# Kernel tuning notes

Measured on AMD Instinct MI355X. Metric: run time of the kernel, lower is better.

## Reference

```python
import jax, jax.numpy as jnp
import numpy as np

D_MODEL = 256
NUM_TYPES = 7
B, N = 2, 512


def setup_inputs() -> dict:
    key = jax.random.key(0)
    k1, k2, k3 = jax.random.split(key, 3)
    lane_features = jax.random.normal(k1, (B, N, D_MODEL), dtype=jnp.float32)
    # nn.Linear(2D, D): weight [D, 2D], bias [D]; stored transposed for x @ W
    s1 = 1.0 / np.sqrt(2 * D_MODEL)
    W1 = jax.random.uniform(k2, (2 * D_MODEL, D_MODEL), minval=-s1, maxval=s1, dtype=jnp.float32)
    b1 = jnp.zeros((D_MODEL,), dtype=jnp.float32)
    s2 = 1.0 / np.sqrt(D_MODEL)
    W2 = jax.random.uniform(k3, (D_MODEL, NUM_TYPES), minval=-s2, maxval=s2, dtype=jnp.float32)
    b2 = jnp.zeros((NUM_TYPES,), dtype=jnp.float32)
    return {"lane_features": lane_features, "W1": W1, "b1": b1, "W2": W2, "b2": b2}


def reference(lane_features, W1, b1, W2, b2):
    # cat([lane_i, lane_j]) @ W1 == lane_i @ W1[:D] + lane_j @ W1[D:]
    D = lane_features.shape[-1]
    W1a, W1b = W1[:D], W1[D:]
    hi = lane_features @ W1a            # [B, N, D]
    hj = lane_features @ W1b            # [B, N, D]
    h = hi[:, :, None, :] + hj[:, None, :, :] + b1  # [B, N, N, D]
    h = jax.nn.relu(h)                  # dropout is identity at inference
    logits = h @ W2 + b2                # [B, N, N, NUM_TYPES]
    return logits
```

## Files before the change

kernel.cpp:

```cpp
#include <hip/hip_runtime.h>

#define D_MODEL   256
#define NUM_TYPES 7
#define BATCH     2
#define NLANES    512
#define LSTR      264

typedef _Float16  f16x8   __attribute__((ext_vector_type(8)));
typedef float     floatx4 __attribute__((ext_vector_type(4)));


__global__ __launch_bounds__(256) void k1_mfma(
    const float* __restrict__ x, const float* __restrict__ W1,
    const float* __restrict__ b1, const float* __restrict__ W2,
    _Float16* __restrict__ Hi16, _Float16* __restrict__ Hj16,
    _Float16* __restrict__ w2f)
{
    const int tid  = threadIdx.x, lane = tid & 63, w = tid >> 6;
    const int nt   = blockIdx.x;
    const int half = nt >> 4;
    const int nc   = (nt & 15) * 16;
    const int m0   = (blockIdx.y * 4 + w) * 16;
    const int jr   = lane & 15, g = lane >> 4, ks = g * 8;

    const float* xrow = x + (size_t)(m0 + jr) * D_MODEL + ks;
    const float* wb   = W1 + (size_t)(half * D_MODEL + ks) * D_MODEL + nc + jr;

    floatx4 acc = {0.f, 0.f, 0.f, 0.f};
    #pragma unroll
    for (int kc = 0; kc < 8; ++kc) {
        const float4 qa = *(const float4*)(xrow + kc * 32);
        const float4 qb = *(const float4*)(xrow + kc * 32 + 4);
        f16x8 a, bfr;
        a[0] = (_Float16)qa.x; a[1] = (_Float16)qa.y;
        a[2] = (_Float16)qa.z; a[3] = (_Float16)qa.w;
        a[4] = (_Float16)qb.x; a[5] = (_Float16)qb.y;
        a[6] = (_Float16)qb.z; a[7] = (_Float16)qb.w;
        const float* wp = wb + (size_t)(kc * 32) * D_MODEL;
        #pragma unroll
        for (int e = 0; e < 8; ++e)
            bfr[e] = (_Float16)wp[(size_t)e * D_MODEL];
        acc = __builtin_amdgcn_mfma_f32_16x16x32_f16(a, bfr, acc, 0, 0, 0);
    }

    _Float16* Hb = half ? Hj16 : Hi16;
    const float bias = half ? 0.f : b1[nc + jr];
    #pragma unroll
    for (int r = 0; r < 4; ++r)
        Hb[(size_t)(m0 + g * 4 + r) * D_MODEL + nc + jr] = (_Float16)(acc[r] + bias);

    if (nt == 0 && blockIdx.y == 0) {
        #pragma unroll
        for (int s0 = 0; s0 < 2; ++s0) {
            const int s   = tid + s0 * 256;
            const int l2  = s & 63, kc2 = s >> 6;
            const int t2  = l2 & 15, ks2 = (l2 >> 4) * 8;
            f16x8 frag;
            #pragma unroll
            for (int e = 0; e < 8; ++e) {
                const int k = kc2 * 32 + ks2 + e;
                frag[e] = (t2 < NUM_TYPES)
                    ? (_Float16)W2[(size_t)k * NUM_TYPES + t2] : (_Float16)0.f;
            }
            *(f16x8*)(w2f + (size_t)s * 8) = frag;
        }
    }
}

#define COMPUTE_U(H, U)                                                          \
    do {                                                                         \
        _Pragma("unroll")                                                        \
        for (int kc = 0; kc < 4; ++kc) {                                         \
            const f16x8 z = {};                                                  \
            f16x8 s0 = __builtin_elementwise_max(H[kc] + hjr0[kc], z);           \
            acc##U[0] = __builtin_amdgcn_mfma_f32_16x16x32_f16(                  \
                w2h[kc], s0, acc##U[0], 0, 0, 0);                                \
            f16x8 s1 = __builtin_elementwise_max(H[kc] + hjr1[kc], z);           \
            acc##U[1] = __builtin_amdgcn_mfma_f32_16x16x32_f16(                  \
                w2h[kc], s1, acc##U[1], 0, 0, 0);                                \
        }                                                                        \
    } while (0)

__global__ __launch_bounds__(256, 4) void k2_pair(
    const _Float16* __restrict__ Hi16, const _Float16* __restrict__ Hj16,
    const _Float16* __restrict__ w2f, const float* __restrict__ b2,
    float* __restrict__ out)
{
    __shared__ _Float16 hs[48][LSTR];

    const int tid  = threadIdx.x;
    const int lane = tid & 63, w = tid >> 6;
    const int b    = blockIdx.z;
    const int j0   = blockIdx.x * 32;
    const int i0   = blockIdx.y * 16;
    const int jr   = lane & 15, g = lane >> 4, ks = g * 8;

    #pragma unroll
    for (int q = 0; q < 2; ++q) {
        const int gg = tid + q * 256;
        const int r  = gg >> 5;
        const int c  = (gg & 31) * 8;
        *(f16x8*)&hs[r][c] = *(const f16x8*)(
            Hi16 + (size_t)(b * NLANES + i0 + r) * D_MODEL + c);
    }
    #pragma unroll
    for (int q = 0; q < 4; ++q) {
        const int gg = tid + q * 256;
        const int r  = gg >> 5;
        const int c  = (gg & 31) * 8;
        *(f16x8*)&hs[16 + r][c] = *(const f16x8*)(
            Hj16 + (size_t)(b * NLANES + j0 + r) * D_MODEL + c);
    }

    const int tb = g * 4;
    float bias2[4];
    #pragma unroll
    for (int r = 0; r < 4; ++r)
        bias2[r] = (tb + r < NUM_TYPES) ? b2[tb + r] : 0.f;

    __syncthreads();

    const int ig = w;
    const f16x8* w2fp = (const f16x8*)w2f + lane;

    floatx4 acc0[2], acc1[2], acc2[2], acc3[2];
    #pragma unroll
    for (int jg = 0; jg < 2; ++jg) {
        acc0[jg] = (floatx4){0.f, 0.f, 0.f, 0.f};
        acc1[jg] = (floatx4){0.f, 0.f, 0.f, 0.f};
        acc2[jg] = (floatx4){0.f, 0.f, 0.f, 0.f};
        acc3[jg] = (floatx4){0.f, 0.f, 0.f, 0.f};
    }

    #pragma unroll
    for (int kch = 0; kch < 2; ++kch) {
        const int kb = kch * 128;

        f16x8 w2h[4];
        #pragma unroll
        for (int kc = 0; kc < 4; ++kc)
            w2h[kc] = w2fp[(kch * 4 + kc) * 64];

        f16x8 hjr0[4], hjr1[4];
        #pragma unroll
        for (int kc = 0; kc < 4; ++kc) {
            hjr0[kc] = *(const f16x8*)&hs[16 + jr][kb + kc * 32 + ks];
            hjr1[kc] = *(const f16x8*)&hs[32 + jr][kb + kc * 32 + ks];
        }

        f16x8 hA[4], hB[4];
        #pragma unroll
        for (int kc = 0; kc < 4; ++kc)
            hA[kc] = *(const f16x8*)&hs[ig * 4 + 0][kb + kc * 32 + ks];
        #pragma unroll
        for (int kc = 0; kc < 4; ++kc)
            hB[kc] = *(const f16x8*)&hs[ig * 4 + 1][kb + kc * 32 + ks];

        COMPUTE_U(hA, 0);
        #pragma unroll
        for (int kc = 0; kc < 4; ++kc)
            hA[kc] = *(const f16x8*)&hs[ig * 4 + 2][kb + kc * 32 + ks];
        COMPUTE_U(hB, 1);
        #pragma unroll
        for (int kc = 0; kc < 4; ++kc)
            hB[kc] = *(const f16x8*)&hs[ig * 4 + 3][kb + kc * 32 + ks];
        COMPUTE_U(hA, 2);
        COMPUTE_U(hB, 3);
    }

    if (lane < 32) {
        floatx4* accs[4] = {acc0, acc1, acc2, acc3};
        #pragma unroll
        for (int u = 0; u < 4; ++u) {
            const int i = i0 + ig * 4 + u;
            #pragma unroll
            for (int jg = 0; jg < 2; ++jg) {
                const floatx4 a = accs[u][jg];
                const int j = j0 + jg * 16 + jr;
                float* op = out + ((size_t)(b * NLANES + i) * NLANES + j) * NUM_TYPES + tb;
                if (tb == 0) {
                    float v4[4] = { a[0] + bias2[0], a[1] + bias2[1],
                                    a[2] + bias2[2], a[3] + bias2[3] };
                    __builtin_memcpy(op, v4, 16);
                } else {
                    float v2[2] = { a[0] + bias2[0], a[1] + bias2[1] };
                    __builtin_memcpy(op, v2, 8);
                    op[2] = a[2] + bias2[2];
                }
            }
        }
    }
}

extern "C" void kernel_launch(void* const* d_in, const int* in_sizes, int n_in,
                              void* d_out, int out_size, void* d_ws, size_t ws_size,
                              hipStream_t stream) {
    const float* x  = (const float*)d_in[0];
    const float* W1 = (const float*)d_in[1];
    const float* b1 = (const float*)d_in[2];
    const float* W2 = (const float*)d_in[3];
    const float* b2 = (const float*)d_in[4];
    float* out = (float*)d_out;

    char* ws = (char*)d_ws;
    _Float16* Hi16 = (_Float16*)ws;
    _Float16* Hj16 = (_Float16*)(ws + 512u * 1024u);
    _Float16* w2f  = (_Float16*)(ws + 1024u * 1024u);

    k1_mfma<<<dim3(32, 16), 256, 0, stream>>>(x, W1, b1, W2, Hi16, Hj16, w2f);
    k2_pair<<<dim3(NLANES / 32, NLANES / 16, BATCH), 256, 0, stream>>>(
        Hi16, Hj16, w2f, b2, out);
}
```

Measured before the change: 22.61 us.

## Read Hi rows from global, keep W2 in registers, loop over j-groups

The pair kernel now stages only the Hj tile in shared memory. Hi rows are loaded directly from global memory per wave, which is lower LDS traffic and a smaller shared footprint. All eight W2 fragments are preloaded into registers, and the loop is restructured to iterate over j-groups with interleaved loads and MFMAs, storing outputs per group. This reduces live accumulators, but Hi rows are now re-read from global or L2 for each j-group, and the extra W2 registers raise register pressure.

```diff
diff --git a/kernel.cpp b/kernel.cpp
--- a/kernel.cpp
+++ b/kernel.cpp
@@ -67,26 +67,12 @@
     }
 }
 
-#define COMPUTE_U(H, U)                                                          \
-    do {                                                                         \
-        _Pragma("unroll")                                                        \
-        for (int kc = 0; kc < 4; ++kc) {                                         \
-            const f16x8 z = {};                                                  \
-            f16x8 s0 = __builtin_elementwise_max(H[kc] + hjr0[kc], z);           \
-            acc##U[0] = __builtin_amdgcn_mfma_f32_16x16x32_f16(                  \
-                w2h[kc], s0, acc##U[0], 0, 0, 0);                                \
-            f16x8 s1 = __builtin_elementwise_max(H[kc] + hjr1[kc], z);           \
-            acc##U[1] = __builtin_amdgcn_mfma_f32_16x16x32_f16(                  \
-                w2h[kc], s1, acc##U[1], 0, 0, 0);                                \
-        }                                                                        \
-    } while (0)
-
 __global__ __launch_bounds__(256, 4) void k2_pair(
     const _Float16* __restrict__ Hi16, const _Float16* __restrict__ Hj16,
     const _Float16* __restrict__ w2f, const float* __restrict__ b2,
     float* __restrict__ out)
 {
-    __shared__ _Float16 hs[48][LSTR];
+    __shared__ __align__(16) _Float16 hjs[32][LSTR];
 
     const int tid  = threadIdx.x;
     const int lane = tid & 63, w = tid >> 6;
@@ -96,21 +82,19 @@
     const int jr   = lane & 15, g = lane >> 4, ks = g * 8;
 
     #pragma unroll
-    for (int q = 0; q < 2; ++q) {
-        const int gg = tid + q * 256;
-        const int r  = gg >> 5;
-        const int c  = (gg & 31) * 8;
-        *(f16x8*)&hs[r][c] = *(const f16x8*)(
-            Hi16 + (size_t)(b * NLANES + i0 + r) * D_MODEL + c);
-    }
-    #pragma unroll
     for (int q = 0; q < 4; ++q) {
         const int gg = tid + q * 256;
         const int r  = gg >> 5;
         const int c  = (gg & 31) * 8;
-        *(f16x8*)&hs[16 + r][c] = *(const f16x8*)(
+        *(f16x8*)&hjs[r][c] = *(const f16x8*)(
             Hj16 + (size_t)(b * NLANES + j0 + r) * D_MODEL + c);
     }
+
+    const f16x8* w2fp = (const f16x8*)w2f + lane;
+    f16x8 w2r[8];
+    #pragma unroll
+    for (int kc = 0; kc < 8; ++kc)
+        w2r[kc] = w2fp[kc * 64];
 
     const int tb = g * 4;
     float bias2[4];
@@ -121,75 +105,68 @@
     __syncthreads();
 
     const int ig = w;
-    const f16x8* w2fp = (const f16x8*)w2f + lane;
+    const _Float16* hiBase = Hi16 + (size_t)(b * NLANES + i0 + ig * 4) * D_MODEL + ks;
 
-    floatx4 acc0[2], acc1[2], acc2[2], acc3[2];
+#define LOAD_HI(DST, U, KB)                                                     \
+    do { _Pragma("unroll") for (int kc = 0; kc < 4; ++kc)                       \
+        DST[kc] = *(const f16x8*)(hiBase + (size_t)(U) * D_MODEL + (KB) + kc * 32); \
+    } while (0)
+
+#define LOAD_HJ(DST, JG, KB)                                                    \
+    do { _Pragma("unroll") for (int kc = 0; kc < 4; ++kc)                       \
+        DST[kc] = *(const f16x8*)&hjs[(JG) * 16 + jr][(KB) + kc * 32 + ks];     \
+    } while (0)
+
+#define COMPUTE_U(HI, HJ, ACC, KH)                                              \
+    do { _Pragma("unroll") for (int kc = 0; kc < 4; ++kc) {                     \
+        const f16x8 z = {};                                                     \
+        f16x8 s = __builtin_elementwise_max(HI[kc] + HJ[kc], z);                \
+        ACC = __builtin_amdgcn_mfma_f32_16x16x32_f16(                           \
+            w2r[(KH) * 4 + kc], s, ACC, 0, 0, 0);                               \
+    } } while (0)
+
     #pragma unroll
     for (int jg = 0; jg < 2; ++jg) {
-        acc0[jg] = (floatx4){0.f, 0.f, 0.f, 0.f};
-        acc1[jg] = (floatx4){0.f, 0.f, 0.f, 0.f};
-        acc2[jg] = (floatx4){0.f, 0.f, 0.f, 0.f};
-        acc3[jg] = (floatx4){0.f, 0.f, 0.f, 0.f};
-    }
+        floatx4 acc0 = {0.f,0.f,0.f,0.f}, acc1 = {0.f,0.f,0.f,0.f};
+        floatx4 acc2 = {0.f,0.f,0.f,0.f}, acc3 = {0.f,0.f,0.f,0.f};
+        f16x8 hjrA[4], hjrB[4], hA[4], hB[4];
 
-    #pragma unroll
-    for (int kch = 0; kch < 2; ++kch) {
-        const int kb = kch * 128;
+        LOAD_HJ(hjrA, jg, 0);
+        LOAD_HI(hA, 0, 0);
+        LOAD_HI(hB, 1, 0);
 
-        f16x8 w2h[4];
-        #pragma unroll
-        for (int kc = 0; kc < 4; ++kc)
-            w2h[kc] = w2fp[(kch * 4 + kc) * 64];
+        COMPUTE_U(hA, hjrA, acc0, 0);  LOAD_HI(hA, 2, 0);
+        COMPUTE_U(hB, hjrA, acc1, 0);  LOAD_HI(hB, 3, 0);
+        LOAD_HJ(hjrB, jg, 128);
+        COMPUTE_U(hA, hjrA, acc2, 0);  LOAD_HI(hA, 0, 128);
+        COMPUTE_U(hB, hjrA, acc3, 0);  LOAD_HI(hB, 1, 128);
+        COMPUTE_U(hA, hjrB, acc0, 1);  LOAD_HI(hA, 2, 128);
+        COMPUTE_U(hB, hjrB, acc1, 1);  LOAD_HI(hB, 3, 128);
+        COMPUTE_U(hA, hjrB, acc2, 1);
+        COMPUTE_U(hB, hjrB, acc3, 1);
 
-        f16x8 hjr0[4], hjr1[4];
-        #pragma unroll
-        for (int kc = 0; kc < 4; ++kc) {
-            hjr0[kc] = *(const f16x8*)&hs[16 + jr][kb + kc * 32 + ks];
-            hjr1[kc] = *(const f16x8*)&hs[32 + jr][kb + kc * 32 + ks];
-        }
-
-        f16x8 hA[4], hB[4];
-        #pragma unroll
-        for (int kc = 0; kc < 4; ++kc)
-            hA[kc] = *(const f16x8*)&hs[ig * 4 + 0][kb + kc * 32 + ks];
-        #pragma unroll
-        for (int kc = 0; kc < 4; ++kc)
-            hB[kc] = *(const f16x8*)&hs[ig * 4 + 1][kb + kc * 32 + ks];
-
-        COMPUTE_U(hA, 0);
-        #pragma unroll
-        for (int kc = 0; kc < 4; ++kc)
-            hA[kc] = *(const f16x8*)&hs[ig * 4 + 2][kb + kc * 32 + ks];
-        COMPUTE_U(hB, 1);
-        #pragma unroll
-        for (int kc = 0; kc < 4; ++kc)
-            hB[kc] = *(const f16x8*)&hs[ig * 4 + 3][kb + kc * 32 + ks];
-        COMPUTE_U(hA, 2);
-        COMPUTE_U(hB, 3);
-    }
-
-    if (lane < 32) {
-        floatx4* accs[4] = {acc0, acc1, acc2, acc3};
-        #pragma unroll
-        for (int u = 0; u < 4; ++u) {
-            const int i = i0 + ig * 4 + u;
+        if (lane < 32) {
+            const floatx4 av[4] = {acc0, acc1, acc2, acc3};
             #pragma unroll
-            for (int jg = 0; jg < 2; ++jg) {
-                const floatx4 a = accs[u][jg];
+            for (int u = 0; u < 4; ++u) {
+                const int i = i0 + ig * 4 + u;
                 const int j = j0 + jg * 16 + jr;
                 float* op = out + ((size_t)(b * NLANES + i) * NLANES + j) * NUM_TYPES + tb;
                 if (tb == 0) {
-                    float v4[4] = { a[0] + bias2[0], a[1] + bias2[1],
-                                    a[2] + bias2[2], a[3] + bias2[3] };
+                    float v4[4] = { av[u][0] + bias2[0], av[u][1] + bias2[1],
+                                    av[u][2] + bias2[2], av[u][3] + bias2[3] };
                     __builtin_memcpy(op, v4, 16);
                 } else {
-                    float v2[2] = { a[0] + bias2[0], a[1] + bias2[1] };
+                    float v2[2] = { av[u][0] + bias2[0], av[u][1] + bias2[1] };
                     __builtin_memcpy(op, v2, 8);
-                    op[2] = a[2] + bias2[2];
+                    op[2] = av[u][2] + bias2[2];
                 }
             }
         }
     }
+#undef LOAD_HI
+#undef LOAD_HJ
+#undef COMPUTE_U
 }
 
 extern "C" void kernel_launch(void* const* d_in, const int* in_sizes, int n_in,
```

New measurement: 40.23 us. +78.0%, slower.
